# Optimization experiments

Measured on AMD Instinct MI355X. Metric: run time of the kernel, lower is better.

## Reference

```python
import jax, jax.numpy as jnp
import numpy as np

H, W = 512, 512          # cart_size
HP, WP = 64, 2048        # polar_size
DROP = 3.0               # center_drop_grid_size
B, C = 4, 64


def _build_grids():
    # Mirrors Polar2Cart.__init__ (mode='in') exactly.
    yy, xx = np.meshgrid(np.arange(H, dtype=np.float32), np.arange(W, dtype=np.float32), indexing='ij')
    yyc = yy - H / 2.0 + 0.5
    xxc = xx - W / 2.0 + 0.5
    depth = np.sqrt(xxc ** 2 + yyc ** 2)
    phi = np.pi - np.arctan2(yyc, xxc)
    index_y = depth / (H / 2.0 * np.sqrt(2.0)) * (HP + DROP) - DROP
    index_x = phi / np.pi / 2.0 * WP
    mask = (index_y > 0).reshape(-1)
    gy = (index_y / HP * 2.0 - 1.0).reshape(-1)[mask]
    gx = (index_x / WP * 2.0 - 1.0).reshape(-1)[mask]
    iy = yy.reshape(-1)[mask].astype(np.int32)
    ix = xx.reshape(-1)[mask].astype(np.int32)
    # torch code stacks (index_x, -index_y) as (x, y) grid coords
    return gx.astype(np.float32), (-gy).astype(np.float32), iy, ix


def setup_inputs() -> dict:
    key = jax.random.key(0)
    k1, k2 = jax.random.split(key)
    gx, gy, iy, ix = _build_grids()
    return {
        'polar_feat': jax.random.normal(k1, (B, C, HP, WP), jnp.float32),
        'ref_feat': jax.random.normal(k2, (B, C, H, W), jnp.float32),
        'grid_x': jnp.asarray(gx),
        'grid_y': jnp.asarray(gy),
        'idx_y': jnp.asarray(iy),
        'idx_x': jnp.asarray(ix),
    }


def _bilinear_sample(feat, gx, gy):
    # feat: [B,C,Hp,Wp]; gx,gy: [N] normalized coords.
    # torch F.grid_sample(mode='bilinear', padding_mode='zeros', align_corners=True)
    Hp, Wp = feat.shape[2], feat.shape[3]
    ixf = (gx + 1.0) * (Wp - 1) * 0.5
    iyf = (gy + 1.0) * (Hp - 1) * 0.5
    x0 = jnp.floor(ixf)
    y0 = jnp.floor(iyf)
    wx1 = ixf - x0
    wy1 = iyf - y0
    out = jnp.zeros((feat.shape[0], feat.shape[1], gx.shape[0]), feat.dtype)
    for dy, wy in ((0, 1.0 - wy1), (1, wy1)):
        for dx, wx in ((0, 1.0 - wx1), (1, wx1)):
            xi = x0 + dx
            yi = y0 + dy
            valid = (xi >= 0) & (xi < Wp) & (yi >= 0) & (yi < Hp)
            xc = jnp.clip(xi, 0, Wp - 1).astype(jnp.int32)
            yc = jnp.clip(yi, 0, Hp - 1).astype(jnp.int32)
            w = jnp.where(valid, wx * wy, 0.0).astype(feat.dtype)
            out = out + feat[:, :, yc, xc] * w  # [B,C,N]
    return out


def reference(polar_feat, ref_feat, grid_x, grid_y, idx_y, idx_x):
    Bc, Cc = ref_feat.shape[0], ref_feat.shape[1]
    N = idx_y.shape[0]
    sampled = _bilinear_sample(polar_feat, grid_x, grid_y)      # [B,C,N]
    vals = sampled.transpose(0, 2, 1).reshape(Bc * N, Cc)       # permute(0,2,1,3).reshape(-1,C)
    b_idx = jnp.repeat(jnp.arange(Bc, dtype=jnp.int32), N)
    out = ref_feat.at[b_idx, :, jnp.tile(idx_y, Bc), jnp.tile(idx_x, Bc)].set(vals)
    return out
```

## Files before the change

kernel.cpp:

```cpp
#include <hip/hip_runtime.h>

#define HH  512
#define WW  512
#define HPP 64
#define WPP 2048
#define BB  4
#define CC  64

__global__ __launch_bounds__(256) void fill_disk(
    const float* __restrict__ ref, float* __restrict__ out) {
    int t  = blockIdx.x * 256 + threadIdx.x;
    int bc = blockIdx.y;
    int r = 240 + (t >> 5);
    int c = 240 + (t & 31);
    float yyc = (float)r - 255.5f;
    float xxc = (float)c - 255.5f;
    float depth = sqrtf(yyc * yyc + xxc * xxc);
    float iyv = depth * (67.0f / 362.03867196751236f) - 3.0f;
    if (iyv <= 1e-3f) {
        size_t off = (size_t)bc * (HH * WW) + (size_t)r * WW + c;
        out[off] = ref[off];
    }
}

__global__ __launch_bounds__(256) void scatter_map(
    const float* __restrict__ gx, const float* __restrict__ gy,
    const int* __restrict__ idx_y, const int* __restrict__ idx_x,
    float2* __restrict__ map, int N) {
    int n = blockIdx.x * 256 + threadIdx.x;
    if (n >= N) return;
    map[idx_y[n] * WW + idx_x[n]] = make_float2(gx[n], gy[n]);
}

struct __attribute__((packed, aligned(4))) fpair { float lo, hi; };

__global__ __launch_bounds__(256) void sample_tiled(
    const float* __restrict__ polar, const float2* __restrict__ map,
    float* __restrict__ out) {
    int bid = blockIdx.x;
    int swz = ((bid & 7) << 7) + (bid >> 3);
    int tile_r = swz >> 5, tile_c = swz & 31;

    int t = (int)threadIdx.x;
    int wave = t >> 6, lane = t & 63;
    int r = tile_r * 16 + ((wave >> 1) << 3) + (lane >> 3);
    int c = tile_c * 16 + ((wave & 1) << 3) + (lane & 7);

    float2 mv = map[r * WW + c];
    if (!(mv.x > -2.0f)) return;
    int b = blockIdx.y;

    float gxv = mv.x, gyv = mv.y;
    float ixf = (gxv + 1.0f) * ((WPP - 1) * 0.5f);
    float iyf = (gyv + 1.0f) * ((HPP - 1) * 0.5f);
    float x0f = floorf(ixf), y0f = floorf(iyf);
    float wx1 = ixf - x0f,  wy1 = iyf - y0f;
    float wx0 = 1.0f - wx1, wy0 = 1.0f - wy1;
    int x0 = (int)x0f, y0 = (int)y0f;
    int x1 = x0 + 1,   y1 = y0 + 1;

    bool vx0 = (x0 >= 0) & (x0 < WPP);
    bool vx1 = (x1 >= 0) & (x1 < WPP);
    bool vy0 = (y0 >= 0) & (y0 < HPP);
    bool vy1 = (y1 >= 0) & (y1 < HPP);
    float w00 = (vx0 && vy0) ? wx0 * wy0 : 0.0f;
    float w01 = (vx1 && vy0) ? wx1 * wy0 : 0.0f;
    float w10 = (vx0 && vy1) ? wx0 * wy1 : 0.0f;
    float w11 = (vx1 && vy1) ? wx1 * wy1 : 0.0f;

    int xs  = min(max(x0, 0), WPP - 2);
    int ys0 = min(max(y0, 0), HPP - 1);
    int ys1 = min(max(y1, 0), HPP - 1);

    const char* pb = (const char*)polar + (size_t)b * ((size_t)CC * HPP * WPP * 4);
    char*       ob = (char*)out + (size_t)b * ((size_t)CC * HH * WW * 4)
                               + (size_t)(r * WW + c) * 4;
    unsigned offA = (unsigned)(ys0 * WPP + xs) * 4u;
    unsigned offB = (unsigned)(ys1 * WPP + xs) * 4u;

    #pragma unroll 8
    for (int ch = 0; ch < CC; ++ch) {
        fpair a01 = *(const fpair*)(pb + offA);
        fpair b01 = *(const fpair*)(pb + offB);
        float v = a01.lo * w00 + a01.hi * w01 + b01.lo * w10 + b01.hi * w11;
        *(float*)ob = v;
        pb += (size_t)HPP * WPP * 4;
        ob += (size_t)HH * WW * 4;
    }
}

__global__ __launch_bounds__(256) void sample_scatter_v2(
    const float* __restrict__ polar,
    const float* __restrict__ gx, const float* __restrict__ gy,
    const int* __restrict__ idx_y, const int* __restrict__ idx_x,
    float* __restrict__ out, int N) {
    int nwg = gridDim.x;
    int bid = blockIdx.x;
    int q = nwg >> 3, rr = nwg & 7;
    int xcd = bid & 7, lid = bid >> 3;
    int swz = (xcd < rr ? xcd * (q + 1) : rr * (q + 1) + (xcd - rr) * q) + lid;

    int n = swz * 256 + (int)threadIdx.x;
    if (n >= N) return;
    int b = blockIdx.y;

    float gxv = gx[n], gyv = gy[n];
    float ixf = (gxv + 1.0f) * ((WPP - 1) * 0.5f);
    float iyf = (gyv + 1.0f) * ((HPP - 1) * 0.5f);
    float x0f = floorf(ixf), y0f = floorf(iyf);
    float wx1 = ixf - x0f,  wy1 = iyf - y0f;
    float wx0 = 1.0f - wx1, wy0 = 1.0f - wy1;
    int x0 = (int)x0f, y0 = (int)y0f;
    int x1 = x0 + 1,   y1 = y0 + 1;

    bool vx0 = (x0 >= 0) & (x0 < WPP);
    bool vx1 = (x1 >= 0) & (x1 < WPP);
    bool vy0 = (y0 >= 0) & (y0 < HPP);
    bool vy1 = (y1 >= 0) & (y1 < HPP);
    float w00 = (vx0 && vy0) ? wx0 * wy0 : 0.0f;
    float w01 = (vx1 && vy0) ? wx1 * wy0 : 0.0f;
    float w10 = (vx0 && vy1) ? wx0 * wy1 : 0.0f;
    float w11 = (vx1 && vy1) ? wx1 * wy1 : 0.0f;

    int xs  = min(max(x0, 0), WPP - 2);
    int ys0 = min(max(y0, 0), HPP - 1);
    int ys1 = min(max(y1, 0), HPP - 1);

    int oy = idx_y[n], ox = idx_x[n];
    const char* pb = (const char*)polar + (size_t)b * ((size_t)CC * HPP * WPP * 4);
    char*       ob = (char*)out + (size_t)b * ((size_t)CC * HH * WW * 4)
                               + (size_t)(oy * WW + ox) * 4;
    unsigned offA = (unsigned)(ys0 * WPP + xs) * 4u;
    unsigned offB = (unsigned)(ys1 * WPP + xs) * 4u;

    #pragma unroll 8
    for (int ch = 0; ch < CC; ++ch) {
        fpair a01 = *(const fpair*)(pb + offA);
        fpair b01 = *(const fpair*)(pb + offB);
        float v = a01.lo * w00 + a01.hi * w01 + b01.lo * w10 + b01.hi * w11;
        __builtin_nontemporal_store(v, (float*)ob);
        pb += (size_t)HPP * WPP * 4;
        ob += (size_t)HH * WW * 4;
    }
}

extern "C" void kernel_launch(void* const* d_in, const int* in_sizes, int n_in,
                              void* d_out, int out_size, void* d_ws, size_t ws_size,
                              hipStream_t stream) {
    const float* polar = (const float*)d_in[0];
    const float* ref   = (const float*)d_in[1];
    const float* gxp   = (const float*)d_in[2];
    const float* gyp   = (const float*)d_in[3];
    const int*   iyp   = (const int*)d_in[4];
    const int*   ixp   = (const int*)d_in[5];
    float* out = (float*)d_out;
    int N = in_sizes[2];

    const size_t map_bytes = (size_t)HH * WW * sizeof(float2);

    fill_disk<<<dim3(4, BB * CC), 256, 0, stream>>>(ref, out);

    if (ws_size >= map_bytes) {
        float2* map = (float2*)d_ws;
        hipMemsetAsync(map, 0xFF, map_bytes, stream);
        scatter_map<<<dim3((N + 255) / 256), 256, 0, stream>>>(
            gxp, gyp, iyp, ixp, map, N);
        sample_tiled<<<dim3(1024, BB), 256, 0, stream>>>(polar, map, out);
    } else {
        sample_scatter_v2<<<dim3((N + 255) / 256, BB), 256, 0, stream>>>(
            polar, gxp, gyp, iyp, ixp, out, N);
    }
}
```

Baseline: 610.7 us.

## Stage per-tile polar footprint in LDS before bilinear sampling

Each 16x16 output tile computes the bounding box of its polar sample coordinates with a wave shuffle plus a block reduction, then, per channel, cooperatively loads that footprint (up to 8 rows by 128 columns) into shared memory and does the bilinear taps from LDS. The aim is to turn scattered, overlapping 8-byte global gathers into coalesced row loads with reuse across neighbouring pixels. Tiles whose footprint is too large fall back to the old direct-gather path. This adds two barriers per channel and a reduction prologue, and tiles near the centre or with a wide angular span may take the fallback anyway.

```diff
diff --git a/kernel.cpp b/kernel.cpp
--- a/kernel.cpp
+++ b/kernel.cpp
@@ -34,31 +34,31 @@
 
 struct __attribute__((packed, aligned(4))) fpair { float lo, hi; };
 
-__global__ __launch_bounds__(256) void sample_tiled(
+__global__ __launch_bounds__(256) void sample_tiled_lds(
     const float* __restrict__ polar, const float2* __restrict__ map,
     float* __restrict__ out) {
+    __shared__ float sbuf[8 * 129];
+    __shared__ int   red[4][4];
+
     int bid = blockIdx.x;
     int swz = ((bid & 7) << 7) + (bid >> 3);
     int tile_r = swz >> 5, tile_c = swz & 31;
 
     int t = (int)threadIdx.x;
-    int wave = t >> 6, lane = t & 63;
-    int r = tile_r * 16 + ((wave >> 1) << 3) + (lane >> 3);
-    int c = tile_c * 16 + ((wave & 1) << 3) + (lane & 7);
+    int wave = t >> 6;
+    int pr = t >> 4, pc = t & 15;
+    int r = tile_r * 16 + pr, c = tile_c * 16 + pc;
 
     float2 mv = map[r * WW + c];
-    if (!(mv.x > -2.0f)) return;
-    int b = blockIdx.y;
-
-    float gxv = mv.x, gyv = mv.y;
-    float ixf = (gxv + 1.0f) * ((WPP - 1) * 0.5f);
-    float iyf = (gyv + 1.0f) * ((HPP - 1) * 0.5f);
+    bool valid = (mv.x > -2.0f);
+
+    float ixf = (mv.x + 1.0f) * ((WPP - 1) * 0.5f);
+    float iyf = (mv.y + 1.0f) * ((HPP - 1) * 0.5f);
     float x0f = floorf(ixf), y0f = floorf(iyf);
     float wx1 = ixf - x0f,  wy1 = iyf - y0f;
     float wx0 = 1.0f - wx1, wy0 = 1.0f - wy1;
     int x0 = (int)x0f, y0 = (int)y0f;
     int x1 = x0 + 1,   y1 = y0 + 1;
-
     bool vx0 = (x0 >= 0) & (x0 < WPP);
     bool vx1 = (x1 >= 0) & (x1 < WPP);
     bool vy0 = (y0 >= 0) & (y0 < HPP);
@@ -68,24 +68,90 @@
     float w10 = (vx0 && vy1) ? wx0 * wy1 : 0.0f;
     float w11 = (vx1 && vy1) ? wx1 * wy1 : 0.0f;
 
-    int xs  = min(max(x0, 0), WPP - 2);
-    int ys0 = min(max(y0, 0), HPP - 1);
-    int ys1 = min(max(y1, 0), HPP - 1);
-
-    const char* pb = (const char*)polar + (size_t)b * ((size_t)CC * HPP * WPP * 4);
-    char*       ob = (char*)out + (size_t)b * ((size_t)CC * HH * WW * 4)
-                               + (size_t)(r * WW + c) * 4;
-    unsigned offA = (unsigned)(ys0 * WPP + xs) * 4u;
-    unsigned offB = (unsigned)(ys1 * WPP + xs) * 4u;
-
-    #pragma unroll 8
-    for (int ch = 0; ch < CC; ++ch) {
-        fpair a01 = *(const fpair*)(pb + offA);
-        fpair b01 = *(const fpair*)(pb + offB);
-        float v = a01.lo * w00 + a01.hi * w01 + b01.lo * w10 + b01.hi * w11;
-        *(float*)ob = v;
-        pb += (size_t)HPP * WPP * 4;
-        ob += (size_t)HH * WW * 4;
+    int rxn = valid ? x0 : INT_MAX, rxm = valid ? x0 : INT_MIN;
+    int ryn = valid ? y0 : INT_MAX, rym = valid ? y0 : INT_MIN;
+    for (int off = 32; off; off >>= 1) {
+        rxn = min(rxn, __shfl_xor(rxn, off));
+        rxm = max(rxm, __shfl_xor(rxm, off));
+        ryn = min(ryn, __shfl_xor(ryn, off));
+        rym = max(rym, __shfl_xor(rym, off));
+    }
+    if ((t & 63) == 0) {
+        red[wave][0] = rxn; red[wave][1] = rxm;
+        red[wave][2] = ryn; red[wave][3] = rym;
+    }
+    __syncthreads();
+    int xmn = min(min(red[0][0], red[1][0]), min(red[2][0], red[3][0]));
+    int xmx = max(max(red[0][1], red[1][1]), max(red[2][1], red[3][1]));
+    int ymn = min(min(red[0][2], red[1][2]), min(red[2][2], red[3][2]));
+    int ymx = max(max(red[0][3], red[1][3]), max(red[2][3], red[3][3]));
+    if (xmn == INT_MAX) return;
+
+    int sxmin = xmn, sxmax = min(xmx + 1, WPP - 1);
+    int symin = ymn, symax = ymx + 1;
+    int ncols = sxmax - sxmin + 1, nrows = symax - symin + 1;
+
+    int b = blockIdx.y;
+    const float* pf = polar + (size_t)b * ((size_t)CC * HPP * WPP);
+    char* ob = (char*)out + (size_t)b * ((size_t)CC * HH * WW * 4)
+                          + (size_t)(r * WW + c) * 4;
+
+    if (nrows <= 8 && ncols <= 128) {
+        int n = nrows * ncols;
+        int gofs[4], lofs[4], cnt = 0;
+        for (int i = t; i < n; i += 256) {
+            int row = i / ncols, col = i - row * ncols;
+            gofs[cnt] = (symin + row) * WPP + sxmin + col;
+            lofs[cnt] = row * 129 + col;
+            ++cnt;
+        }
+        int lx0 = 0, lx1 = 0, ly0 = 0, ly1 = 0;
+        if (valid) {
+            lx0 = x0 - sxmin;
+            lx1 = min(lx0 + 1, ncols - 1);
+            ly0 = y0 - symin; ly1 = ly0 + 1;
+        }
+        int a00 = ly0 * 129 + lx0, a01 = ly0 * 129 + lx1;
+        int a10 = ly1 * 129 + lx0, a11 = ly1 * 129 + lx1;
+
+        for (int ch = 0; ch < CC; ++ch) {
+            __syncthreads();
+            float v0, v1, v2, v3;
+            if (cnt > 0) v0 = pf[gofs[0]];
+            if (cnt > 1) v1 = pf[gofs[1]];
+            if (cnt > 2) v2 = pf[gofs[2]];
+            if (cnt > 3) v3 = pf[gofs[3]];
+            if (cnt > 0) sbuf[lofs[0]] = v0;
+            if (cnt > 1) sbuf[lofs[1]] = v1;
+            if (cnt > 2) sbuf[lofs[2]] = v2;
+            if (cnt > 3) sbuf[lofs[3]] = v3;
+            __syncthreads();
+            if (valid) {
+                float p00 = sbuf[a00], p01 = sbuf[a01];
+                float p10 = sbuf[a10], p11 = sbuf[a11];
+                float v = p00 * w00 + p01 * w01 + p10 * w10 + p11 * w11;
+                *(float*)ob = v;
+            }
+            pf += HPP * WPP;
+            ob += (size_t)HH * WW * 4;
+        }
+    } else {
+        if (!valid) return;
+        int xs  = min(max(x0, 0), WPP - 2);
+        int ys0 = min(max(y0, 0), HPP - 1);
+        int ys1 = min(max(y1, 0), HPP - 1);
+        unsigned offA = (unsigned)(ys0 * WPP + xs) * 4u;
+        unsigned offB = (unsigned)(ys1 * WPP + xs) * 4u;
+        const char* pb = (const char*)pf;
+        #pragma unroll 8
+        for (int ch = 0; ch < CC; ++ch) {
+            fpair a01 = *(const fpair*)(pb + offA);
+            fpair b01 = *(const fpair*)(pb + offB);
+            float v = a01.lo * w00 + a01.hi * w01 + b01.lo * w10 + b01.hi * w11;
+            *(float*)ob = v;
+            pb += (size_t)HPP * WPP * 4;
+            ob += (size_t)HH * WW * 4;
+        }
     }
 }
 
@@ -165,7 +231,7 @@
         hipMemsetAsync(map, 0xFF, map_bytes, stream);
         scatter_map<<<dim3((N + 255) / 256), 256, 0, stream>>>(
             gxp, gyp, iyp, ixp, map, N);
-        sample_tiled<<<dim3(1024, BB), 256, 0, stream>>>(polar, map, out);
+        sample_tiled_lds<<<dim3(1024, BB), 256, 0, stream>>>(polar, map, out);
     } else {
         sample_scatter_v2<<<dim3((N + 255) / 256, BB), 256, 0, stream>>>(
             polar, gxp, gyp, iyp, ixp, out, N);
```

After: 637.5 us. 1.04x slower.
